# Performance work log

Hardware: AMD Instinct MI355X
Metric: run time of the kernel (lower is better)

Reference implementation:

```python
import jax, jax.numpy as jnp
import numpy as np

V, D, L, H, HD, S = 50257, 768, 8, 6, 128, 2048
BS = 128          # flex-attention BLOCK_SIZE
EOS = 50256       # document separator token
EPS = 1.1920929e-07  # torch F.rms_norm default eps (f32 machine eps)
ATTN_SCALE = 0.12


def rms(x):
    return x * jax.lax.rsqrt(jnp.mean(jnp.square(x), axis=-1, keepdims=True) + EPS)


def rope_tables(seq_len, hd):
    # modded-nanogpt rotary: hd//4 geometric freqs + hd//4 zero freqs, applied to half-split dims
    freqs = (1.0 / 1024.0) ** jnp.linspace(0.0, 1.0, hd // 4)
    freqs = jnp.concatenate([freqs, jnp.zeros(hd // 4, dtype=jnp.float32)])
    theta = jnp.arange(seq_len, dtype=jnp.float32)[:, None] * freqs[None, :]  # [S, hd//2]
    return jnp.cos(theta), jnp.sin(theta)


def rope(x, cos, sin):  # x: [B,S,H,hd]
    x1, x2 = jnp.split(x, 2, axis=-1)
    c = cos[None, :, None, :]
    s = sin[None, :, None, :]
    return jnp.concatenate([x1 * c + x2 * s, -x1 * s + x2 * c], axis=-1)


def build_token_mask(input_seq, w):
    # Reproduces BlockMask.from_kv_blocks semantics: per query-row keep the w-1 most
    # recent FULL blocks and min(n_partial, max(w - n_full, 1)) most recent PARTIAL
    # blocks; mask_mod (document-causal) applies inside partial blocks only.
    NB = S // BS
    docs = jnp.cumsum((input_seq == EOS).astype(jnp.int32))
    bi = jnp.arange(NB)
    dr = docs.reshape(NB, BS)
    dl, dh = dr[:, 0], dr[:, -1]
    m_any = (bi[:, None] >= bi[None, :]) & (dl[:, None] <= dh[None, :]) & (dh[:, None] >= dl[None, :])
    m_all = (bi[:, None] > bi[None, :]) & (dl[:, None] == dh[None, :]) & (dh[:, None] == dl[None, :])
    part = m_any & ~m_all
    nf = m_all.sum(-1)

    def keep_most_recent(m, kcount):  # keep kcount True entries with largest kv index
        r = jnp.cumsum(m[:, ::-1].astype(jnp.int32), axis=-1)[:, ::-1]
        return m & (r <= kcount[:, None])

    kf = keep_most_recent(m_all, jnp.minimum(nf, w - 1))
    kp = keep_most_recent(part, jnp.minimum(part.sum(-1), jnp.maximum(w - nf, 1)))
    tf = jnp.repeat(jnp.repeat(kf, BS, 0), BS, 1)   # [S,S]
    tp = jnp.repeat(jnp.repeat(kp, BS, 0), BS, 1)
    q = jnp.arange(S)
    tok = (q[:, None] >= q[None, :]) & (docs[:, None] == docs[None, :])
    return tf | (tp & tok)


def _forward(input_seq, sliding_window_num_blocks, target_seq, embed, ve_embeds,
             qkv_w, attn_proj_w, mlp_fc_w, mlp_proj_w, scalars):
    cos, sin = rope_tables(S, HD)
    long_m = build_token_mask(input_seq, sliding_window_num_blocks)
    short_m = build_token_mask(input_seq, sliding_window_num_blocks // 2)
    cycle = [long_m, short_m, short_m, short_m]
    masks = (cycle * ((L + 3) // 4))[:L - 1] + [long_m]

    ve_tok = ve_embeds[:, input_seq, :]  # [3,S,D]
    ve = [ve_tok[0], ve_tok[1], ve_tok[2]] + [None] * (L - 6) + [ve_tok[0], ve_tok[1], ve_tok[2]]

    skip_w = scalars[:L]
    lambdas = scalars[L:3 * L].reshape(L, 2)
    sa_lambdas = scalars[3 * L:5 * L].reshape(L, 2)

    stride = max(1, L // 4)
    skip_map = {}
    for m in range(3):
        i = L - 3 + m
        j = i - stride * (m + 1)
        if 0 <= j < i < L:
            skip_map[i] = j

    x = x0 = rms(embed[input_seq])[None]  # [1,S,D]
    skips = []
    for i in range(L):
        if i in skip_map:
            x = x + skip_w[skip_map[i]] * skips[skip_map[i]]
        lam, sal = lambdas[i], sa_lambdas[i]
        # Block: residual mix with x0, attn, mlp (modded-nanogpt style)
        x = lam[0] * x + lam[1] * x0
        xa = rms(x)
        qkv = (xa @ qkv_w[i].T).reshape(1, S, 3 * H, HD)
        q, k, v = jnp.split(qkv, 3, axis=2)
        q = rope(rms(q), cos, sin)
        k = rope(rms(k), cos, sin)
        if ve[i] is not None:
            v = sal[0] * v + sal[1] * ve[i].reshape(1, S, H, HD)
        else:
            v = sal[0] * v
        scores = jnp.einsum('bqhd,bkhd->bhqk', q, k) * ATTN_SCALE
        scores = jnp.where(masks[i][None, None], scores, -jnp.inf)
        y = jnp.einsum('bhqk,bkhd->bqhd', jax.nn.softmax(scores, axis=-1), v)
        x = x + y.reshape(1, S, H * HD) @ attn_proj_w[i].T
        h = jnp.square(jax.nn.relu(rms(x) @ mlp_fc_w[i].T))
        x = x + h @ mlp_proj_w[i].T
        skips.append(x)

    x = rms(x)
    logits = (x[0].astype(jnp.bfloat16) @ embed.T.astype(jnp.bfloat16)).astype(jnp.float32)
    cap = 15.0 * logits * jax.lax.rsqrt(jnp.square(logits) + 225.0)  # softcap
    lsm = jax.nn.log_softmax(cap, axis=-1)
    return -jnp.mean(lsm[jnp.arange(S), target_seq])


def setup_inputs() -> dict:
    key = jax.random.key(0)
    ks = jax.random.split(key, 9)
    input_seq = jax.random.randint(ks[0], (S,), 0, V)
    input_seq = input_seq.at[jnp.arange(0, S, 512)].set(EOS)  # inject doc boundaries
    target_seq = jax.random.randint(ks[1], (S,), 0, V)
    embed = jax.random.normal(ks[2], (V, D), jnp.float32)
    ve_embeds = jax.random.normal(ks[3], (3, V, D), jnp.float32)
    sd = 1.0 / np.sqrt(D)
    qkv_w = jax.random.normal(ks[4], (L, 3 * H * HD, D), jnp.float32) * sd
    attn_proj_w = jax.random.normal(ks[5], (L, D, H * HD), jnp.float32) * (1.0 / np.sqrt(H * HD))
    mlp_fc_w = jax.random.normal(ks[6], (L, 4 * D, D), jnp.float32) * sd
    mlp_proj_w = jax.random.normal(ks[7], (L, D, 4 * D), jnp.float32) * (1.0 / np.sqrt(4 * D))
    scalars = jnp.concatenate([
        jnp.ones(L), jnp.tile(jnp.array([1.0, 0.0]), L), jnp.tile(jnp.array([0.5, 0.5]), L)
    ]).astype(jnp.float32) + 0.02 * jax.random.normal(ks[8], (5 * L,), jnp.float32)
    return {"input_seq": input_seq, "sliding_window_num_blocks": 8, "target_seq": target_seq,
            "embed": embed, "ve_embeds": ve_embeds, "qkv_w": qkv_w, "attn_proj_w": attn_proj_w,
            "mlp_fc_w": mlp_fc_w, "mlp_proj_w": mlp_proj_w, "scalars": scalars}


def reference(input_seq, sliding_window_num_blocks, target_seq, embed, ve_embeds,
              qkv_w, attn_proj_w, mlp_fc_w, mlp_proj_w, scalars):
    return _forward(input_seq, sliding_window_num_blocks, target_seq, embed, ve_embeds,
                    qkv_w, attn_proj_w, mlp_fc_w, mlp_proj_w, scalars)
```

## Files before the change

### kernel.cpp

```cpp
#include <hip/hip_runtime.h>
#include <hip/hip_bf16.h>
#include <math.h>

#define NSEQ 2048
#define NDIM 768
#define NLAY 8
#define NHEAD 6
#define NHD 128
#define NVOC 50257
#define NBLK 16
#define BLKSZ 128
#define EOS_TOK 50256
#define EPSF 1.1920929e-07f
#define ASCALE 0.12f
#define NVT 393

#define GSWZ(r) (((r) ^ ((r) >> 2)) & 3)

using bf16x8 = __attribute__((ext_vector_type(8))) __bf16;
using bf16x4 = __attribute__((ext_vector_type(4))) __bf16;
using f32x4  = __attribute__((ext_vector_type(4))) float;

__device__ __forceinline__ __bf16 tobf(float x) {
  __hip_bfloat16 h = __float2bfloat16(x);
  return *reinterpret_cast<__bf16*>(&h);
}

__global__ __launch_bounds__(256) void cvt_bf16_kernel(const float* __restrict__ in, __bf16* __restrict__ out,
                                                       long n) {
  long i = ((long)blockIdx.x * blockDim.x + threadIdx.x) * 4;
  long stride = (long)gridDim.x * blockDim.x * 4;
  for (; i < n; i += stride) {
    float4 v = *(const float4*)(in + i);
    bf16x4 o;
    o[0] = tobf(v.x); o[1] = tobf(v.y); o[2] = tobf(v.z); o[3] = tobf(v.w);
    *(bf16x4*)(out + i) = o;
  }
}

__global__ __launch_bounds__(1024) void prep_kernel(const int* __restrict__ seq, const int* __restrict__ wptr,
                                                    int* __restrict__ docs, int* __restrict__ catL,
                                                    int* __restrict__ catS) {
  __shared__ int f[NSEQ];
  __shared__ int g[NSEQ];
  int tid = threadIdx.x;
  for (int i = tid; i < NSEQ; i += 1024) f[i] = (seq[i] == EOS_TOK) ? 1 : 0;
  __syncthreads();
  int* a = f; int* b = g;
  for (int off = 1; off < NSEQ; off <<= 1) {
    for (int i = tid; i < NSEQ; i += 1024) {
      int v = a[i];
      if (i >= off) v += a[i - off];
      b[i] = v;
    }
    __syncthreads();
    int* t = a; a = b; b = t;
  }
  for (int i = tid; i < NSEQ; i += 1024) docs[i] = a[i];
  __syncthreads();
  if (tid == 0) {
    int dl[NBLK], dh[NBLK];
    for (int bi = 0; bi < NBLK; ++bi) { dl[bi] = a[bi * BLKSZ]; dh[bi] = a[bi * BLKSZ + BLKSZ - 1]; }
    int W = *wptr;
    for (int pass = 0; pass < 2; ++pass) {
      int w = (pass == 0) ? W : (W / 2);
      int* cat = (pass == 0) ? catL : catS;
      for (int i = 0; i < NBLK; ++i) {
        int allr[NBLK], partr[NBLK];
        int nf = 0, np = 0;
        for (int j = 0; j < NBLK; ++j) {
          int any_ = (i >= j) && (dl[i] <= dh[j]) && (dh[i] >= dl[j]);
          int all_ = (i > j) && (dl[i] == dh[j]) && (dh[i] == dl[j]);
          allr[j] = all_; partr[j] = any_ && !all_;
          nf += all_; np += partr[j];
        }
        int kcf = min(nf, w - 1);
        int kcp = min(np, max(w - nf, 1));
        int cf = 0, cp = 0;
        for (int j = NBLK - 1; j >= 0; --j) {
          int cv = 0;
          if (allr[j]) { cf++; if (cf <= kcf) cv = 2; }
          if (partr[j]) { cp++; if (cp <= kcp) cv = 1; }
          cat[i * NBLK + j] = cv;
        }
      }
    }
  }
}

__global__ __launch_bounds__(256) void embed_rms_kernel(const int* __restrict__ seq, const float* __restrict__ embed,
                                                        float* __restrict__ x, float* __restrict__ x0) {
  int s = blockIdx.x;
  int tid = threadIdx.x;
  const float* row = embed + (size_t)seq[s] * NDIM;
  float v0 = row[tid], v1 = row[tid + 256], v2 = row[tid + 512];
  float ss = v0 * v0 + v1 * v1 + v2 * v2;
  __shared__ float red[256];
  red[tid] = ss; __syncthreads();
  for (int o = 128; o > 0; o >>= 1) { if (tid < o) red[tid] += red[tid + o]; __syncthreads(); }
  float sc = rsqrtf(red[0] / (float)NDIM + EPSF);
  size_t base = (size_t)s * NDIM;
  float o0 = v0 * sc, o1 = v1 * sc, o2 = v2 * sc;
  x[base + tid] = o0; x[base + tid + 256] = o1; x[base + tid + 512] = o2;
  x0[base + tid] = o0; x0[base + tid + 256] = o1; x0[base + tid + 512] = o2;
}

__global__ __launch_bounds__(256) void rmsbf_kernel(const float* __restrict__ x, __bf16* __restrict__ xb) {
  int s = blockIdx.x;
  int tid = threadIdx.x;
  size_t base = (size_t)s * NDIM;
  float v0 = x[base + tid], v1 = x[base + tid + 256], v2 = x[base + tid + 512];
  float ss = v0 * v0 + v1 * v1 + v2 * v2;
  __shared__ float red[256];
  red[tid] = ss; __syncthreads();
  for (int o = 128; o > 0; o >>= 1) { if (tid < o) red[tid] += red[tid + o]; __syncthreads(); }
  float sc = rsqrtf(red[0] / (float)NDIM + EPSF);
  xb[base + tid] = tobf(v0 * sc); xb[base + tid + 256] = tobf(v1 * sc); xb[base + tid + 512] = tobf(v2 * sc);
}

__global__ __launch_bounds__(256) void mixrms_kernel(float* __restrict__ x, const float* __restrict__ x0,
                                                     const float* __restrict__ skip, const float* __restrict__ scal,
                                                     int li, int sj, __bf16* __restrict__ xb) {
  float lam0 = scal[NLAY + 2 * li], lam1 = scal[NLAY + 2 * li + 1];
  float sw = (sj >= 0) ? scal[sj] : 0.f;
  int s = blockIdx.x;
  int tid = threadIdx.x;
  size_t base = (size_t)s * NDIM;
  float xv[3], ov[3], nv[3];
  xv[0] = x[base + tid]; xv[1] = x[base + tid + 256]; xv[2] = x[base + tid + 512];
  ov[0] = x0[base + tid]; ov[1] = x0[base + tid + 256]; ov[2] = x0[base + tid + 512];
  if (skip) {
    nv[0] = lam0 * (xv[0] + sw * skip[base + tid])       + lam1 * ov[0];
    nv[1] = lam0 * (xv[1] + sw * skip[base + tid + 256]) + lam1 * ov[1];
    nv[2] = lam0 * (xv[2] + sw * skip[base + tid + 512]) + lam1 * ov[2];
  } else {
    nv[0] = lam0 * xv[0] + lam1 * ov[0];
    nv[1] = lam0 * xv[1] + lam1 * ov[1];
    nv[2] = lam0 * xv[2] + lam1 * ov[2];
  }
  x[base + tid] = nv[0]; x[base + tid + 256] = nv[1]; x[base + tid + 512] = nv[2];
  float ss = nv[0] * nv[0] + nv[1] * nv[1] + nv[2] * nv[2];
  __shared__ float red[256];
  red[tid] = ss; __syncthreads();
  for (int o = 128; o > 0; o >>= 1) { if (tid < o) red[tid] += red[tid + o]; __syncthreads(); }
  float sc = rsqrtf(red[0] / (float)NDIM + EPSF);
  xb[base + tid] = tobf(nv[0] * sc); xb[base + tid + 256] = tobf(nv[1] * sc); xb[base + tid + 512] = tobf(nv[2] * sc);
}

template <int MODE>
__global__ __launch_bounds__(256) void gemm_mfma(const __bf16* __restrict__ A, const __bf16* __restrict__ B,
                                                 float* __restrict__ Cf, __bf16* __restrict__ Cb,
                                                 int N, int K) {
  __shared__ __bf16 As[2][128 * 32];
  __shared__ __bf16 Bs[2][128 * 32];
  int bm = blockIdx.x * 128, bn = blockIdx.y * 128;
  int tid = threadIdx.x;
  int w = tid >> 6, l = tid & 63;
  int wm = (w >> 1) * 64, wn = (w & 1) * 64;
  int c = l & 15, g = l >> 4;

  auto stage = [&](int buf, int k0) {
#pragma unroll
    for (int i = 0; i < 2; ++i) {
      int L = (w * 2 + i) * 64 + l;
      int row = L >> 2, gc = L & 3;
      int gs = gc ^ GSWZ(row);
      const __bf16* srcA = A + (size_t)(bm + row) * K + k0 + gs * 8;
      const __bf16* srcB = B + (size_t)(bn + row) * K + k0 + gs * 8;
      __builtin_amdgcn_global_load_lds(
          (const __attribute__((address_space(1))) void*)srcA,
          (__attribute__((address_space(3))) void*)&As[buf][(w * 2 + i) * 512], 16, 0, 0);
      __builtin_amdgcn_global_load_lds(
          (const __attribute__((address_space(1))) void*)srcB,
          (__attribute__((address_space(3))) void*)&Bs[buf][(w * 2 + i) * 512], 16, 0, 0);
    }
  };

  f32x4 acc[4][4] = {};
  stage(0, 0);
  __syncthreads();
  int nk = K >> 5;
  for (int kk = 0; kk < nk; ++kk) {
    int buf = kk & 1;
    if (kk + 1 < nk) stage(buf ^ 1, (kk + 1) * 32);
    bf16x8 af[4], bfr[4];
#pragma unroll
    for (int i = 0; i < 4; ++i) {
      int row = wm + i * 16 + c;
      af[i] = *(const bf16x8*)&As[buf][row * 32 + (g ^ GSWZ(row)) * 8];
    }
#pragma unroll
    for (int j = 0; j < 4; ++j) {
      int row = wn + j * 16 + c;
      bfr[j] = *(const bf16x8*)&Bs[buf][row * 32 + (g ^ GSWZ(row)) * 8];
    }
#pragma unroll
    for (int i = 0; i < 4; ++i)
#pragma unroll
      for (int j = 0; j < 4; ++j)
        acc[i][j] = __builtin_amdgcn_mfma_f32_16x16x32_bf16(af[i], bfr[j], acc[i][j], 0, 0, 0);
    __syncthreads();
  }
#pragma unroll
  for (int i = 0; i < 4; ++i)
#pragma unroll
    for (int j = 0; j < 4; ++j)
#pragma unroll
      for (int rr = 0; rr < 4; ++rr) {
        int row = bm + wm + i * 16 + g * 4 + rr;
        int col = bn + wn + j * 16 + c;
        size_t ci = (size_t)row * N + col;
        float z = acc[i][j][rr];
        if (MODE == 0) Cf[ci] = z;
        else if (MODE == 1) Cf[ci] += z;
        else { float r = fmaxf(z, 0.f); Cb[ci] = tobf(r * r); }
      }
}

template <int MODE>
__global__ __launch_bounds__(256) void gemm_mfma64(const __bf16* __restrict__ A, const __bf16* __restrict__ B,
                                                   float* __restrict__ Cf, __bf16* __restrict__ Cb,
                                                   int N, int K) {
  __shared__ __bf16 As[2][64 * 32];
  __shared__ __bf16 Bs[2][64 * 32];
  int bm = blockIdx.x * 64, bn = blockIdx.y * 64;
  int tid = threadIdx.x;
  int w = tid >> 6, l = tid & 63;
  int wm = (w >> 1) * 32, wn = (w & 1) * 32;
  int c = l & 15, g = l >> 4;

  auto stage = [&](int buf, int k0) {
    int L = w * 64 + l;
    int row = L >> 2, gc = L & 3;
    int gs = gc ^ GSWZ(row);
    const __bf16* srcA = A + (size_t)(bm + row) * K + k0 + gs * 8;
    const __bf16* srcB = B + (size_t)(bn + row) * K + k0 + gs * 8;
    __builtin_amdgcn_global_load_lds(
        (const __attribute__((address_space(1))) void*)srcA,
        (__attribute__((address_space(3))) void*)&As[buf][w * 512], 16, 0, 0);
    __builtin_amdgcn_global_load_lds(
        (const __attribute__((address_space(1))) void*)srcB,
        (__attribute__((address_space(3))) void*)&Bs[buf][w * 512], 16, 0, 0);
  };

  f32x4 acc[2][2] = {};
  stage(0, 0);
  __syncthreads();
  int nk = K >> 5;
  for (int kk = 0; kk < nk; ++kk) {
    int buf = kk & 1;
    if (kk + 1 < nk) stage(buf ^ 1, (kk + 1) * 32);
    bf16x8 af[2], bfr[2];
#pragma unroll
    for (int i = 0; i < 2; ++i) {
      int row = wm + i * 16 + c;
      af[i] = *(const bf16x8*)&As[buf][row * 32 + (g ^ GSWZ(row)) * 8];
    }
#pragma unroll
    for (int j = 0; j < 2; ++j) {
      int row = wn + j * 16 + c;
      bfr[j] = *(const bf16x8*)&Bs[buf][row * 32 + (g ^ GSWZ(row)) * 8];
    }
#pragma unroll
    for (int i = 0; i < 2; ++i)
#pragma unroll
      for (int j = 0; j < 2; ++j)
        acc[i][j] = __builtin_amdgcn_mfma_f32_16x16x32_bf16(af[i], bfr[j], acc[i][j], 0, 0, 0);
    __syncthreads();
  }
#pragma unroll
  for (int i = 0; i < 2; ++i)
#pragma unroll
    for (int j = 0; j < 2; ++j)
#pragma unroll
      for (int rr = 0; rr < 4; ++rr) {
        int row = bm + wm + i * 16 + g * 4 + rr;
        int col = bn + wn + j * 16 + c;
        size_t ci = (size_t)row * N + col;
        float z = acc[i][j][rr];
        if (MODE == 0) Cf[ci] = z;
        else if (MODE == 1) Cf[ci] += z;
        else { float r = fmaxf(z, 0.f); Cb[ci] = tobf(r * r); }
      }
}

__global__ __launch_bounds__(256) void qkv_post_kernel(const float* __restrict__ qkv, const float* __restrict__ vemb,
                                                       const int* __restrict__ seq, const float* __restrict__ scal,
                                                       int li, int ve_idx,
                                                       __bf16* __restrict__ qo, __bf16* __restrict__ ko,
                                                       __bf16* __restrict__ vo) {
  int p = blockIdx.x * 4 + (threadIdx.x >> 6);
  int l = threadIdx.x & 63;
  int h = p >> 11;
  int s = p & (NSEQ - 1);
  float sal0 = scal[3 * NLAY + 2 * li], sal1 = scal[3 * NLAY + 2 * li + 1];
  float fr = (l < 32) ? powf(1.0f / 1024.0f, (float)l * (1.0f / 31.0f)) : 0.f;
  float th = (float)s * fr;
  float cth = cosf(th), sth = sinf(th);
  size_t rb = (size_t)s * (3 * NHEAD * NHD) + h * NHD;
  float q0 = qkv[rb + l],                 q1 = qkv[rb + l + 64];
  float k0 = qkv[rb + NHEAD * NHD + l],   k1 = qkv[rb + NHEAD * NHD + l + 64];
  float v0 = qkv[rb + 2 * NHEAD * NHD + l], v1 = qkv[rb + 2 * NHEAD * NHD + l + 64];
  float ssq = q0 * q0 + q1 * q1;
  float ssk = k0 * k0 + k1 * k1;
#pragma unroll
  for (int o = 1; o < 64; o <<= 1) {
    ssq += __shfl_xor(ssq, o, 64);
    ssk += __shfl_xor(ssk, o, 64);
  }
  float scq = rsqrtf(ssq / (float)NHD + EPSF);
  float sck = rsqrtf(ssk / (float)NHD + EPSF);
  float qn0 = q0 * scq, qn1 = q1 * scq;
  float kn0 = k0 * sck, kn1 = k1 * sck;
  float oq0 = qn0 * cth + qn1 * sth, oq1 = -qn0 * sth + qn1 * cth;
  float ok0 = kn0 * cth + kn1 * sth, ok1 = -kn0 * sth + kn1 * cth;
  float ov0 = sal0 * v0, ov1 = sal0 * v1;
  if (ve_idx >= 0) {
    const float* ver = vemb + ((size_t)ve_idx * NVOC + seq[s]) * NDIM + h * NHD;
    ov0 += sal1 * ver[l];
    ov1 += sal1 * ver[l + 64];
  }
  size_t oo = ((size_t)h * NSEQ + s) * NHD;
  qo[oo + l] = tobf(oq0); qo[oo + l + 64] = tobf(oq1);
  ko[oo + l] = tobf(ok0); ko[oo + l + 64] = tobf(ok1);
  vo[oo + l] = tobf(ov0); vo[oo + l + 64] = tobf(ov1);
}

__global__ __launch_bounds__(256) void vtrans_kernel(const __bf16* __restrict__ v, __bf16* __restrict__ vt) {
  int st = blockIdx.x * 64, dt = blockIdx.y * 64, h = blockIdx.z;
  __shared__ __bf16 t[64][65];
  int tid = threadIdx.x;
  for (int e = tid; e < 4096; e += 256) {
    int s = e >> 6, d = e & 63;
    t[s][d] = v[((size_t)h * NSEQ + st + s) * NHD + dt + d];
  }
  __syncthreads();
  for (int e = tid; e < 512; e += 256) {
    int d = e >> 3, s0 = (e & 7) * 8;
    bf16x8 ov;
#pragma unroll
    for (int i = 0; i < 8; ++i) ov[i] = t[s0 + i][d];
    *(bf16x8*)(vt + ((size_t)h * NHD + dt + d) * NSEQ + st + s0) = ov;
  }
}

__global__ __launch_bounds__(128) void attn_mfma_kernel(const __bf16* __restrict__ qb, const __bf16* __restrict__ kb,
                                                        const __bf16* __restrict__ vt, const int* __restrict__ cat,
                                                        const int* __restrict__ docs, __bf16* __restrict__ y) {
  int qb32 = (int)gridDim.x - 1 - (int)blockIdx.x;
  int h = blockIdx.y;
  int tid = threadIdx.x;
  int wq = tid >> 6;
  int l = tid & 63;
  int c = l & 15, g = l >> 4;
  int q0 = qb32 * 32 + wq * 16;
  int qB = qb32 >> 2;

  __shared__ __bf16 Ks[2][32 * 128];
  __shared__ __bf16 Vts[2][32 * 128];
  __shared__ __bf16 Ps[2][16 * 32];
  __shared__ int kvs[64];
  __shared__ int kvc[64];
  __shared__ int nact_s;

  if (tid == 0) {
    int n = 0;
    for (int kv = 0; kv <= qb32; ++kv) {
      int cc = cat[qB * NBLK + (kv >> 2)];
      if (cc) { kvs[n] = kv; kvc[n] = cc; ++n; }
    }
    nact_s = n;
  }

  bf16x8 qf[4];
#pragma unroll
  for (int ks = 0; ks < 4; ++ks)
    qf[ks] = *(const bf16x8*)(qb + ((size_t)h * NSEQ + q0 + c) * NHD + ks * 32 + g * 8);

  int qd[4];
#pragma unroll
  for (int rr = 0; rr < 4; ++rr) qd[rr] = docs[q0 + g * 4 + rr];

  float m[4], lden[4];
#pragma unroll
  for (int rr = 0; rr < 4; ++rr) { m[rr] = -INFINITY; lden[rr] = 0.f; }
  f32x4 oacc[8] = {};

  __syncthreads();
  int nact = nact_s;

  auto stage = [&](int kv, int bufi) {
#pragma unroll
    for (int i = 0; i < 4; ++i) {
      int L = (wq * 4 + i) * 64 + l;
      int krow = L >> 4, gl = L & 15;
      int gs = gl ^ (krow & 7);
      const __bf16* srcK = kb + ((size_t)h * NSEQ + kv * 32 + krow) * NHD + gs * 8;
      __builtin_amdgcn_global_load_lds(
          (const __attribute__((address_space(1))) void*)srcK,
          (__attribute__((address_space(3))) void*)&Ks[bufi][(wq * 4 + i) * 512], 16, 0, 0);
      int drow = L >> 2, gk = L & 3;
      const __bf16* srcV = vt + ((size_t)h * NHD + drow) * NSEQ + kv * 32 + gk * 8;
      __builtin_amdgcn_global_load_lds(
          (const __attribute__((address_space(1))) void*)srcV,
          (__attribute__((address_space(3))) void*)&Vts[bufi][(wq * 4 + i) * 512], 16, 0, 0);
    }
  };

  stage(kvs[0], 0);
  __syncthreads();

  for (int it = 0; it < nact; ++it) {
    int buf = it & 1;
    if (it + 1 < nact) stage(kvs[it + 1], buf ^ 1);
    int kv = kvs[it], cc = kvc[it];
    int k0 = kv * 32;

    f32x4 sacc[2] = {};
#pragma unroll
    for (int ks = 0; ks < 4; ++ks) {
#pragma unroll
      for (int j = 0; j < 2; ++j) {
        int row = j * 16 + c;
        int gi = (ks * 4 + g) ^ (row & 7);
        bf16x8 kf = *(const bf16x8*)&Ks[buf][row * 128 + gi * 8];
        sacc[j] = __builtin_amdgcn_mfma_f32_16x16x32_bf16(qf[ks], kf, sacc[j], 0, 0, 0);
      }
    }
    float sc[2][4];
    float bmax[4] = {-INFINITY, -INFINITY, -INFINITY, -INFINITY};
#pragma unroll
    for (int j = 0; j < 2; ++j) {
      int key = k0 + j * 16 + c;
      int kdj = docs[key];
#pragma unroll
      for (int rr = 0; rr < 4; ++rr) {
        int qrow = q0 + g * 4 + rr;
        bool ok = (cc == 2) || ((key <= qrow) && (kdj == qd[rr]));
        float z = ok ? sacc[j][rr] * ASCALE : -INFINITY;
        sc[j][rr] = z;
        bmax[rr] = fmaxf(bmax[rr], z);
      }
    }
#pragma unroll
    for (int rr = 0; rr < 4; ++rr) {
      bmax[rr] = fmaxf(bmax[rr], __shfl_xor(bmax[rr], 1, 64));
      bmax[rr] = fmaxf(bmax[rr], __shfl_xor(bmax[rr], 2, 64));
      bmax[rr] = fmaxf(bmax[rr], __shfl_xor(bmax[rr], 4, 64));
      bmax[rr] = fmaxf(bmax[rr], __shfl_xor(bmax[rr], 8, 64));
    }
    float corr[4], psum[4];
#pragma unroll
    for (int rr = 0; rr < 4; ++rr) {
      float mnew = fmaxf(m[rr], bmax[rr]);
      float msafe = (mnew == -INFINITY) ? 0.f : mnew;
      corr[rr] = __expf(m[rr] - msafe);
      float p0 = __expf(sc[0][rr] - msafe);
      float p1 = __expf(sc[1][rr] - msafe);
      sc[0][rr] = p0; sc[1][rr] = p1;
      psum[rr] = p0 + p1;
      m[rr] = mnew;
    }
#pragma unroll
    for (int rr = 0; rr < 4; ++rr) {
      psum[rr] += __shfl_xor(psum[rr], 1, 64);
      psum[rr] += __shfl_xor(psum[rr], 2, 64);
      psum[rr] += __shfl_xor(psum[rr], 4, 64);
      psum[rr] += __shfl_xor(psum[rr], 8, 64);
      lden[rr] = lden[rr] * corr[rr] + psum[rr];
    }
#pragma unroll
    for (int nt = 0; nt < 8; ++nt)
#pragma unroll
      for (int rr = 0; rr < 4; ++rr) oacc[nt][rr] *= corr[rr];
#pragma unroll
    for (int j = 0; j < 2; ++j)
#pragma unroll
      for (int rr = 0; rr < 4; ++rr)
        Ps[wq][(g * 4 + rr) * 32 + j * 16 + c] = tobf(sc[j][rr]);
    asm volatile("s_waitcnt lgkmcnt(0)" ::: "memory");
    bf16x8 pf = *(const bf16x8*)&Ps[wq][c * 32 + g * 8];
#pragma unroll
    for (int nt = 0; nt < 8; ++nt) {
      bf16x8 vf = *(const bf16x8*)&Vts[buf][(nt * 16 + c) * 32 + g * 8];
      oacc[nt] = __builtin_amdgcn_mfma_f32_16x16x32_bf16(pf, vf, oacc[nt], 0, 0, 0);
    }
    __syncthreads();
  }
  float inv[4];
#pragma unroll
  for (int rr = 0; rr < 4; ++rr) inv[rr] = (lden[rr] > 0.f) ? 1.f / lden[rr] : 0.f;
#pragma unroll
  for (int nt = 0; nt < 8; ++nt)
#pragma unroll
    for (int rr = 0; rr < 4; ++rr) {
      int qrow = q0 + g * 4 + rr;
      y[(size_t)qrow * NDIM + h * NHD + nt * 16 + c] = tobf(oacc[nt][rr] * inv[rr]);
    }
}

__global__ __launch_bounds__(256) void logits_gemm_kernel(const __bf16* __restrict__ xbf,
                                                          const __bf16* __restrict__ embed_bf,
                                                          const int* __restrict__ target,
                                                          float* __restrict__ part_m, float* __restrict__ part_l,
                                                          float* __restrict__ tcap) {
  __shared__ __bf16 As[2][128 * 32];
  __shared__ __bf16 Bs[2][128 * 32];
  __shared__ float rm2[2][128];
  __shared__ float rs2[2][128];
  int bm = blockIdx.x * 128;
  int vt = blockIdx.y;
  int bn = vt * 128;
  int tid = threadIdx.x;
  int w = tid >> 6, l = tid & 63;
  int wm = (w >> 1) * 64, wn = (w & 1) * 64;
  int c = l & 15, g = l >> 4;

  auto stage = [&](int buf, int k0) {
#pragma unroll
    for (int i = 0; i < 2; ++i) {
      int L = (w * 2 + i) * 64 + l;
      int row = L >> 2, gc = L & 3;
      int gs = gc ^ GSWZ(row);
      int vrow = bn + row;
      if (vrow >= NVOC) vrow = NVOC - 1;
      const __bf16* srcA = xbf + (size_t)(bm + row) * NDIM + k0 + gs * 8;
      const __bf16* srcB = embed_bf + (size_t)vrow * NDIM + k0 + gs * 8;
      __builtin_amdgcn_global_load_lds(
          (const __attribute__((address_space(1))) void*)srcA,
          (__attribute__((address_space(3))) void*)&As[buf][(w * 2 + i) * 512], 16, 0, 0);
      __builtin_amdgcn_global_load_lds(
          (const __attribute__((address_space(1))) void*)srcB,
          (__attribute__((address_space(3))) void*)&Bs[buf][(w * 2 + i) * 512], 16, 0, 0);
    }
  };

  f32x4 acc[4][4] = {};
  stage(0, 0);
  __syncthreads();
  const int nk = NDIM / 32;
  for (int kk = 0; kk < nk; ++kk) {
    int buf = kk & 1;
    if (kk + 1 < nk) stage(buf ^ 1, (kk + 1) * 32);
    bf16x8 af[4], bfr[4];
#pragma unroll
    for (int i = 0; i < 4; ++i) {
      int row = wm + i * 16 + c;
      af[i] = *(const bf16x8*)&As[buf][row * 32 + (g ^ GSWZ(row)) * 8];
    }
#pragma unroll
    for (int j = 0; j < 4; ++j) {
      int row = wn + j * 16 + c;
      bfr[j] = *(const bf16x8*)&Bs[buf][row * 32 + (g ^ GSWZ(row)) * 8];
    }
#pragma unroll
    for (int i = 0; i < 4; ++i)
#pragma unroll
      for (int j = 0; j < 4; ++j)
        acc[i][j] = __builtin_amdgcn_mfma_f32_16x16x32_bf16(af[i], bfr[j], acc[i][j], 0, 0, 0);
    __syncthreads();
  }

#pragma unroll
  for (int i = 0; i < 4; ++i) {
#pragma unroll
    for (int rr = 0; rr < 4; ++rr) {
      int rowl = wm + i * 16 + g * 4 + rr;
      int tg = target[bm + rowl];
      float tmax = -INFINITY;
#pragma unroll
      for (int j = 0; j < 4; ++j) {
        int vv = bn + wn + j * 16 + c;
        bool okv = vv < NVOC;
        float z = acc[i][j][rr];
        float cp = okv ? 15.f * z * rsqrtf(z * z + 225.f) : -INFINITY;
        tmax = fmaxf(tmax, cp);
        if (okv && vv == tg) tcap[bm + rowl] = cp;
      }
      tmax = fmaxf(tmax, __shfl_xor(tmax, 1, 64));
      tmax = fmaxf(tmax, __shfl_xor(tmax, 2, 64));
      tmax = fmaxf(tmax, __shfl_xor(tmax, 4, 64));
      tmax = fmaxf(tmax, __shfl_xor(tmax, 8, 64));
      float ts = 0.f;
#pragma unroll
      for (int j = 0; j < 4; ++j) {
        int vv = bn + wn + j * 16 + c;
        bool okv = vv < NVOC;
        float z = acc[i][j][rr];
        float cp = 15.f * z * rsqrtf(z * z + 225.f);
        ts += okv ? __expf(cp - tmax) : 0.f;
      }
      ts += __shfl_xor(ts, 1, 64);
      ts += __shfl_xor(ts, 2, 64);
      ts += __shfl_xor(ts, 4, 64);
      ts += __shfl_xor(ts, 8, 64);
      if (c == 0) { rm2[w & 1][rowl] = tmax; rs2[w & 1][rowl] = ts; }
    }
  }
  __syncthreads();
  if (tid < 128) {
    float m0 = rm2[0][tid], m1 = rm2[1][tid];
    float s0 = rs2[0][tid], s1 = rs2[1][tid];
    float mn = fmaxf(m0, m1);
    float ls = s0 * __expf(m0 - mn) + s1 * __expf(m1 - mn);
    part_m[(size_t)vt * NSEQ + bm + tid] = mn;
    part_l[(size_t)vt * NSEQ + bm + tid] = ls;
  }
}

__global__ __launch_bounds__(256) void lossrow_kernel(const float* __restrict__ part_m, const float* __restrict__ part_l,
                                                      const float* __restrict__ tcap, float* __restrict__ lr) {
  int row = blockIdx.x * 256 + threadIdx.x;
  float M = -INFINITY;
  for (int cc = 0; cc < NVT; ++cc) M = fmaxf(M, part_m[(size_t)cc * NSEQ + row]);
  float L = 0.f;
  for (int cc = 0; cc < NVT; ++cc) L += part_l[(size_t)cc * NSEQ + row] * __expf(part_m[(size_t)cc * NSEQ + row] - M);
  lr[row] = (M + logf(L)) - tcap[row];
}

__global__ __launch_bounds__(256) void loss2_kernel(const float* __restrict__ lr, float* __restrict__ out) {
  int tid = threadIdx.x;
  float sum = 0.f;
  for (int t = tid; t < NSEQ; t += 256) sum += lr[t];
  __shared__ float red[256];
  red[tid] = sum; __syncthreads();
  for (int o = 128; o > 0; o >>= 1) { if (tid < o) red[tid] += red[tid + o]; __syncthreads(); }
  if (tid == 0) out[0] = red[0] / (float)NSEQ;
}

extern "C" void kernel_launch(void* const* d_in, const int* in_sizes, int n_in,
                              void* d_out, int out_size, void* d_ws, size_t ws_size,
                              hipStream_t stream) {
  const int* seq   = (const int*)d_in[0];
  const int* wnb   = (const int*)d_in[1];
  const int* tgt   = (const int*)d_in[2];
  const float* embed = (const float*)d_in[3];
  const float* vemb  = (const float*)d_in[4];
  const float* qkvw  = (const float*)d_in[5];
  const float* aprj  = (const float*)d_in[6];
  const float* fcw   = (const float*)d_in[7];
  const float* prjw  = (const float*)d_in[8];
  const float* scal  = (const float*)d_in[9];
  float* out = (float*)d_out;

  char* w = (char*)d_ws;
  auto alloc = [&](size_t bytes) {
    char* p = w;
    w += (bytes + 255) & ~(size_t)255;
    return p;
  };
  int* docs = (int*)alloc(NSEQ * 4);
  int* catL = (int*)alloc(NBLK * NBLK * 4);
  int* catS = (int*)alloc(NBLK * NBLK * 4);
  float* x    = (float*)alloc((size_t)NSEQ * NDIM * 4);
  float* x0   = (float*)alloc((size_t)NSEQ * NDIM * 4);
  float* sk1  = (float*)alloc((size_t)NSEQ * NDIM * 4);
  float* sk2  = (float*)alloc((size_t)NSEQ * NDIM * 4);
  float* sk3  = (float*)alloc((size_t)NSEQ * NDIM * 4);
  float* qkvb = (float*)alloc((size_t)NSEQ * 3 * NHEAD * NHD * 4);
  __bf16* qbf2 = (__bf16*)alloc((size_t)NHEAD * NSEQ * NHD * 2);
  __bf16* kbf2 = (__bf16*)alloc((size_t)NHEAD * NSEQ * NHD * 2);
  __bf16* vbf2 = (__bf16*)alloc((size_t)NHEAD * NSEQ * NHD * 2);
  __bf16* vtbf = (__bf16*)alloc((size_t)NHEAD * NHD * NSEQ * 2);
  __bf16* xabf = (__bf16*)alloc((size_t)NSEQ * NDIM * 2);
  __bf16* ybf  = (__bf16*)alloc((size_t)NSEQ * NDIM * 2);
  __bf16* hbf  = (__bf16*)alloc((size_t)NSEQ * 4 * NDIM * 2);
  __bf16* xbf  = (__bf16*)alloc((size_t)NSEQ * NDIM * 2);
  float* pm   = (float*)alloc((size_t)NVT * NSEQ * 4);
  float* pl   = (float*)alloc((size_t)NVT * NSEQ * 4);
  float* tc   = (float*)alloc((size_t)NSEQ * 4);
  float* lrow = (float*)alloc((size_t)NSEQ * 4);
  __bf16* embbf = (__bf16*)alloc((size_t)NVOC * NDIM * 2);
  __bf16* qkvwbf = (__bf16*)alloc((size_t)NLAY * 3 * NHEAD * NHD * NDIM * 2);
  __bf16* aprjbf = (__bf16*)alloc((size_t)NLAY * NDIM * NDIM * 2);
  __bf16* fcwbf  = (__bf16*)alloc((size_t)NLAY * 4 * NDIM * NDIM * 2);
  __bf16* prjwbf = (__bf16*)alloc((size_t)NLAY * NDIM * 4 * NDIM * 2);
  float* skips[4] = {nullptr, sk1, sk2, sk3};

  cvt_bf16_kernel<<<2048, 256, 0, stream>>>(embed, embbf, (long)NVOC * NDIM);
  cvt_bf16_kernel<<<2048, 256, 0, stream>>>(qkvw, qkvwbf, (long)NLAY * 3 * NHEAD * NHD * NDIM);
  cvt_bf16_kernel<<<2048, 256, 0, stream>>>(aprj, aprjbf, (long)NLAY * NDIM * NDIM);
  cvt_bf16_kernel<<<2048, 256, 0, stream>>>(fcw, fcwbf, (long)NLAY * 4 * NDIM * NDIM);
  cvt_bf16_kernel<<<2048, 256, 0, stream>>>(prjw, prjwbf, (long)NLAY * NDIM * 4 * NDIM);

  prep_kernel<<<1, 1024, 0, stream>>>(seq, wnb, docs, catL, catS);
  embed_rms_kernel<<<NSEQ, 256, 0, stream>>>(seq, embed, x, x0);

  const int velist[NLAY]   = {0, 1, 2, -1, -1, 0, 1, 2};
  const int skipj[NLAY]    = {-1, -1, -1, -1, -1, 3, 2, 1};
  const int maskLong[NLAY] = {1, 0, 0, 0, 1, 0, 0, 1};

  for (int i = 0; i < NLAY; ++i) {
    mixrms_kernel<<<NSEQ, 256, 0, stream>>>(x, x0, skipj[i] >= 0 ? skips[skipj[i]] : nullptr, scal, i, skipj[i], xabf);
    gemm_mfma<0><<<dim3(NSEQ / 128, (3 * NHEAD * NHD) / 128), 256, 0, stream>>>(
        xabf, qkvwbf + (size_t)i * 3 * NHEAD * NHD * NDIM, qkvb, nullptr, 3 * NHEAD * NHD, NDIM);
    qkv_post_kernel<<<NHEAD * NSEQ / 4, 256, 0, stream>>>(qkvb, vemb, seq, scal, i, velist[i], qbf2, kbf2, vbf2);
    vtrans_kernel<<<dim3(NSEQ / 64, NHD / 64, NHEAD), 256, 0, stream>>>(vbf2, vtbf);
    attn_mfma_kernel<<<dim3(NSEQ / 32, NHEAD), 128, 0, stream>>>(qbf2, kbf2, vtbf, maskLong[i] ? catL : catS, docs, ybf);
    gemm_mfma64<1><<<dim3(NSEQ / 64, NDIM / 64), 256, 0, stream>>>(
        ybf, aprjbf + (size_t)i * NDIM * NDIM, x, nullptr, NDIM, NDIM);
    rmsbf_kernel<<<NSEQ, 256, 0, stream>>>(x, xabf);
    gemm_mfma<2><<<dim3(NSEQ / 128, (4 * NDIM) / 128), 256, 0, stream>>>(
        xabf, fcwbf + (size_t)i * 4 * NDIM * NDIM, nullptr, hbf, 4 * NDIM, NDIM);
    gemm_mfma64<1><<<dim3(NSEQ / 64, NDIM / 64), 256, 0, stream>>>(
        hbf, prjwbf + (size_t)i * NDIM * 4 * NDIM, x, nullptr, NDIM, 4 * NDIM);
    if (i >= 1 && i <= 3) {
      hipMemcpyAsync(skips[i], x, (size_t)NSEQ * NDIM * 4, hipMemcpyDeviceToDevice, stream);
    }
  }

  rmsbf_kernel<<<NSEQ, 256, 0, stream>>>(x, xbf);
  logits_gemm_kernel<<<dim3(NSEQ / 128, NVT), 256, 0, stream>>>(xbf, embbf, tgt, pm, pl, tc);
  lossrow_kernel<<<NSEQ / 256, 256, 0, stream>>>(pm, pl, tc, lrow);
  loss2_kernel<<<1, 256, 0, stream>>>(lrow, out);
}
```

Baseline: 2.005 ms.

## Use fixed softcap bound as softmax shift and remap logits block order

```diff
diff --git a/kernel.cpp b/kernel.cpp
--- a/kernel.cpp
+++ b/kernel.cpp
@@ -14,6 +14,7 @@
 #define EPSF 1.1920929e-07f
 #define ASCALE 0.12f
 #define NVT 393
+#define CAPSH 15.f
 
 #define GSWZ(r) (((r) ^ ((r) >> 2)) & 3)
 
@@ -502,14 +503,15 @@
 __global__ __launch_bounds__(256) void logits_gemm_kernel(const __bf16* __restrict__ xbf,
                                                           const __bf16* __restrict__ embed_bf,
                                                           const int* __restrict__ target,
-                                                          float* __restrict__ part_m, float* __restrict__ part_l,
+                                                          float* __restrict__ part_l,
                                                           float* __restrict__ tcap) {
   __shared__ __bf16 As[2][128 * 32];
   __shared__ __bf16 Bs[2][128 * 32];
-  __shared__ float rm2[2][128];
   __shared__ float rs2[2][128];
-  int bm = blockIdx.x * 128;
-  int vt = blockIdx.y;
+  int lid = (int)blockIdx.y * (int)gridDim.x + (int)blockIdx.x;
+  int nid = (lid & 7) * 786 + (lid >> 3);
+  int bm = (nid & 15) * 128;
+  int vt = nid >> 4;
   int bn = vt * 128;
   int tid = threadIdx.x;
   int w = tid >> 6, l = tid & 63;
@@ -567,20 +569,6 @@
     for (int rr = 0; rr < 4; ++rr) {
       int rowl = wm + i * 16 + g * 4 + rr;
       int tg = target[bm + rowl];
-      float tmax = -INFINITY;
-#pragma unroll
-      for (int j = 0; j < 4; ++j) {
-        int vv = bn + wn + j * 16 + c;
-        bool okv = vv < NVOC;
-        float z = acc[i][j][rr];
-        float cp = okv ? 15.f * z * rsqrtf(z * z + 225.f) : -INFINITY;
-        tmax = fmaxf(tmax, cp);
-        if (okv && vv == tg) tcap[bm + rowl] = cp;
-      }
-      tmax = fmaxf(tmax, __shfl_xor(tmax, 1, 64));
-      tmax = fmaxf(tmax, __shfl_xor(tmax, 2, 64));
-      tmax = fmaxf(tmax, __shfl_xor(tmax, 4, 64));
-      tmax = fmaxf(tmax, __shfl_xor(tmax, 8, 64));
       float ts = 0.f;
 #pragma unroll
       for (int j = 0; j < 4; ++j) {
@@ -588,34 +576,28 @@
         bool okv = vv < NVOC;
         float z = acc[i][j][rr];
         float cp = 15.f * z * rsqrtf(z * z + 225.f);
-        ts += okv ? __expf(cp - tmax) : 0.f;
+        ts += okv ? __expf(cp - CAPSH) : 0.f;
+        if (okv && vv == tg) tcap[bm + rowl] = cp;
       }
       ts += __shfl_xor(ts, 1, 64);
       ts += __shfl_xor(ts, 2, 64);
       ts += __shfl_xor(ts, 4, 64);
       ts += __shfl_xor(ts, 8, 64);
-      if (c == 0) { rm2[w & 1][rowl] = tmax; rs2[w & 1][rowl] = ts; }
+      if (c == 0) rs2[w & 1][rowl] = ts;
     }
   }
   __syncthreads();
   if (tid < 128) {
-    float m0 = rm2[0][tid], m1 = rm2[1][tid];
-    float s0 = rs2[0][tid], s1 = rs2[1][tid];
-    float mn = fmaxf(m0, m1);
-    float ls = s0 * __expf(m0 - mn) + s1 * __expf(m1 - mn);
-    part_m[(size_t)vt * NSEQ + bm + tid] = mn;
-    part_l[(size_t)vt * NSEQ + bm + tid] = ls;
-  }
-}
-
-__global__ __launch_bounds__(256) void lossrow_kernel(const float* __restrict__ part_m, const float* __restrict__ part_l,
+    part_l[(size_t)vt * NSEQ + bm + tid] = rs2[0][tid] + rs2[1][tid];
+  }
+}
+
+__global__ __launch_bounds__(256) void lossrow_kernel(const float* __restrict__ part_l,
                                                       const float* __restrict__ tcap, float* __restrict__ lr) {
   int row = blockIdx.x * 256 + threadIdx.x;
-  float M = -INFINITY;
-  for (int cc = 0; cc < NVT; ++cc) M = fmaxf(M, part_m[(size_t)cc * NSEQ + row]);
   float L = 0.f;
-  for (int cc = 0; cc < NVT; ++cc) L += part_l[(size_t)cc * NSEQ + row] * __expf(part_m[(size_t)cc * NSEQ + row] - M);
-  lr[row] = (M + logf(L)) - tcap[row];
+  for (int cc = 0; cc < NVT; ++cc) L += part_l[(size_t)cc * NSEQ + row];
+  lr[row] = (CAPSH + logf(L)) - tcap[row];
 }
 
 __global__ __launch_bounds__(256) void loss2_kernel(const float* __restrict__ lr, float* __restrict__ out) {
@@ -666,7 +648,6 @@
   __bf16* ybf  = (__bf16*)alloc((size_t)NSEQ * NDIM * 2);
   __bf16* hbf  = (__bf16*)alloc((size_t)NSEQ * 4 * NDIM * 2);
   __bf16* xbf  = (__bf16*)alloc((size_t)NSEQ * NDIM * 2);
-  float* pm   = (float*)alloc((size_t)NVT * NSEQ * 4);
   float* pl   = (float*)alloc((size_t)NVT * NSEQ * 4);
   float* tc   = (float*)alloc((size_t)NSEQ * 4);
   float* lrow = (float*)alloc((size_t)NSEQ * 4);
@@ -710,7 +691,7 @@
   }
 
   rmsbf_kernel<<<NSEQ, 256, 0, stream>>>(x, xbf);
-  logits_gemm_kernel<<<dim3(NSEQ / 128, NVT), 256, 0, stream>>>(xbf, embbf, tgt, pm, pl, tc);
-  lossrow_kernel<<<NSEQ / 256, 256, 0, stream>>>(pm, pl, tc, lrow);
+  logits_gemm_kernel<<<dim3(NSEQ / 128, NVT), 256, 0, stream>>>(xbf, embbf, tgt, pl, tc);
+  lossrow_kernel<<<NSEQ / 256, 256, 0, stream>>>(pl, tc, lrow);
   loss2_kernel<<<1, 256, 0, stream>>>(lrow, out);
 }
```

After: 1.826 ms. 1.1x faster.
